# Optimization experiments

Hardware: AMD Instinct MI355X
Metric: run time of the kernel (lower is better)

## Reference

```python
import jax, jax.numpy as jnp
import numpy as np

B, L, C = 8, 1_000_000, 4


def _spiral_size(length: int) -> int:
    # size = round(sqrt(L / (pi/4 * 0.7)) / 2) * 2 + 1  (odd, size^2 >= L)
    s = np.sqrt(length / (np.pi / 4.0 * 0.7))
    return int(np.round(s / 2.0)) * 2 + 1


def _spiral_perm(size: int, length: int):
    """Grid slot index for each signal position (first `length` of argsort(phi2))."""
    PI = jnp.float32(np.pi)
    rnge = jnp.arange(size, dtype=jnp.float32) - size / 2.0 + 0.5
    x1, x2 = jnp.meshgrid(rnge, rnge)  # 'xy' indexing, same as tf.meshgrid default
    r = jnp.sqrt(x1 * x1 + x2 * x2)
    phi = jnp.arccos(x1 / r)                      # NaN at center (0/0)
    phi = jnp.where(jnp.isnan(phi), 0.0, phi)
    phi = phi * jnp.sign(x2)
    phi = phi + jnp.where((x2 == 0.0) & (x1 < 0.0), PI, 0.0)
    phi2 = jnp.round(r) * 2.0 * PI + phi          # spiral ordering key
    return jnp.argsort(phi2.reshape(-1))[:length]


def setup_inputs() -> dict:
    key = jax.random.key(0)
    return {"inputs": jax.random.normal(key, (B, L, C), dtype=jnp.float32)}


def reference(inputs):
    b, l, c = inputs.shape
    size = _spiral_size(l)
    perm = _spiral_perm(size, l)  # [l] unique grid slots
    # One-pass scatter of the signal into the dense size*size spiral grid
    grid = jnp.zeros((b, size * size, c), dtype=inputs.dtype).at[:, perm, :].set(inputs)
    return grid.reshape(b, size, size, c)
```

## Files before the change

kernel.cpp:

```cpp
#include <hip/hip_runtime.h>
#include <cstdint>

#define SIZE 1349
#define HALF 674
#define N2 (SIZE*SIZE)
#define LSIG 1000000
#define NB 8
#define GRID_RINGS 954
#define RANK_RINGS 600
#define CAP 5376
#define MBUCKET 2048

__device__ __forceinline__ int isqrt_i(int n) {
    int s = (int)sqrtf((float)n);
    while (s > 0 && s * s > n) s--;
    while ((s + 1) * (s + 1) <= n) s++;
    return s;
}

__device__ __forceinline__ int row_interval(int k, int y, int* xlo, int* xhi) {
    if (k == 0) { if (y == 0) { *xhi = 0; return 1; } return 0; }
    int yy = y * y;
    int B = k * (k + 1) - yy;
    if (B < 0) return 0;
    int h = isqrt_i(B);
    if (h > HALF) h = HALF;
    int A = k * (k - 1) + 1 - yy;
    *xhi = h;
    if (A <= 0) return 1;
    int f = isqrt_i(A);
    int lo = (f * f == A) ? f : f + 1;
    if (lo > h) return 0;
    *xlo = lo;
    return 2;
}

__device__ __forceinline__ uint32_t rowcnt(int k, int y) {
    int lo, hi;
    int kind = row_interval(k, y, &lo, &hi);
    if (kind == 0) return 0u;
    if (kind == 1) return (uint32_t)(2 * hi + 1);
    return (uint32_t)(2 * (hi - lo + 1));
}

__global__ void k_prep1(uint32_t* __restrict__ ringCount) {
    __shared__ uint32_t red[256];
    int k = blockIdx.x, t = threadIdx.x;
    int ymaxv = min(k, HALF);
    int nrows = 2 * ymaxv + 1;
    uint32_t s = 0;
    for (int i = t; i < nrows; i += 256) s += rowcnt(k, i - ymaxv);
    red[t] = s;
    __syncthreads();
    for (int d = 128; d > 0; d >>= 1) { if (t < d) red[t] += red[t + d]; __syncthreads(); }
    if (t == 0) ringCount[k] = red[0];
}

__global__ void k_prep2(const uint32_t* __restrict__ ringCount,
                        uint32_t* __restrict__ ringOffset,
                        uint32_t* __restrict__ nthresh) {
    __shared__ uint32_t s[1024];
    int t = threadIdx.x;
    uint32_t mine = (t < RANK_RINGS) ? ringCount[t] : 0u;
    s[t] = mine;
    __syncthreads();
    for (int d = 1; d < 1024; d <<= 1) {
        uint32_t x = (t >= d) ? s[t - d] : 0u;
        __syncthreads();
        s[t] += x;
        __syncthreads();
    }
    if (t < RANK_RINGS) ringOffset[t] = s[t] - mine;
    if (t >= 2 && t < RANK_RINGS && s[t - 1] >= LSIG && s[t - 2] < LSIG)
        *nthresh = (uint32_t)(t * (t - 1) + 1);
}

__device__ __forceinline__ int bucket_of(uint32_t kb, float tt) {
    const float PI_F = 3.14159265358979323846f;
    const float SC = 325.94932f;
    float p2 = __uint_as_float(kb);
    float u = (p2 - tt) + PI_F;
    int b = (int)(u * SC);
    return min(max(b, 0), MBUCKET - 1);
}

template<int PHASE>
__device__ __forceinline__ void enum_ring(int k, int ymaxv, float tt, int t,
                                          uint32_t* cnt, uint32_t* boff, uint64_t* T) {
#pragma clang fp contract(off)
    const float PI_F = 3.14159265358979323846f;
    int ntask = 2 * (ymaxv + 1);
    for (int task = t; task < ntask; task += 1024) {
        int y = task >> 1, side = task & 1;
        int xlo = 0, xhi = 0;
        int kind = row_interval(k, y, &xlo, &xhi);
        if (kind == 0) continue;
        int xs, xe;
        if (side == 0) {
            xs = -xhi; xe = (kind == 1) ? -1 : -xlo;
            if (xe < xs) continue;
        } else {
            xs = (kind == 1) ? 0 : xlo; xe = xhi;
        }
        for (int x = xs; x <= xe; ++x) {
            uint32_t kp, kn = 0;
            if (y == 0) {
                float phi = (x < 0) ? PI_F : 0.0f;
                kp = __float_as_uint(tt + phi);
            } else {
                int nn = x * x + y * y;
                float rr = sqrtf((float)nn);
                float q = (float)x / rr;
                float ac = (float)::acos((double)q);
                kp = __float_as_uint(tt + ac);
                kn = __float_as_uint(tt - ac);
            }
            uint32_t gx = (uint32_t)(x + HALF);
            uint32_t gp = (uint32_t)(y + HALF) * SIZE + gx;
            int bp = bucket_of(kp, tt);
            if (PHASE == 0) atomicAdd(&cnt[bp], 1u);
            else { uint32_t p = atomicAdd(&boff[bp], 1u); T[p] = ((uint64_t)kp << 32) | gp; }
            if (y > 0) {
                uint32_t gn = (uint32_t)(HALF - y) * SIZE + gx;
                int bn = bucket_of(kn, tt);
                if (PHASE == 0) atomicAdd(&cnt[bn], 1u);
                else { uint32_t p = atomicAdd(&boff[bn], 1u); T[p] = ((uint64_t)kn << 32) | gn; }
            }
        }
    }
}

__global__ __launch_bounds__(1024) void k_rank(const uint32_t* __restrict__ ringOffset,
                                               const uint32_t* __restrict__ ringCount,
                                               uint32_t* __restrict__ rank) {
#pragma clang fp contract(off)
    __shared__ uint64_t T[CAP];
    __shared__ uint32_t cnt[MBUCKET];
    __shared__ uint32_t boff[MBUCKET];
    __shared__ uint32_t ps[1024];
    const float PI_F = 3.14159265358979323846f;
    int k = (RANK_RINGS - 1) - blockIdx.x;
    int t = threadIdx.x;
    uint32_t off = ringOffset[k];
    if (off >= LSIG) return;
    if (k == 0) { if (t == 0) rank[HALF * SIZE + HALF] = 0u; return; }
    int ymaxv = min(k, HALF);
    int n = (int)ringCount[k];
    float tt = (2.0f * (float)k) * PI_F;

    cnt[2 * t] = 0u; cnt[2 * t + 1] = 0u;
    __syncthreads();

    enum_ring<0>(k, ymaxv, tt, t, cnt, boff, T);
    __syncthreads();

    uint32_t c0 = cnt[2 * t], c1 = cnt[2 * t + 1];
    uint32_t s = c0 + c1;
    ps[t] = s;
    __syncthreads();
    for (int d = 1; d < 1024; d <<= 1) {
        uint32_t x = (t >= d) ? ps[t - d] : 0u;
        __syncthreads();
        ps[t] += x;
        __syncthreads();
    }
    uint32_t excl = ps[t] - s;
    boff[2 * t] = excl;
    boff[2 * t + 1] = excl + c0;
    __syncthreads();

    enum_ring<1>(k, ymaxv, tt, t, cnt, boff, T);
    __syncthreads();

    for (int i = t; i < n; i += 1024) {
        uint64_t v = T[i];
        uint32_t kb = (uint32_t)(v >> 32);
        int b = bucket_of(kb, tt);
        uint32_t end = boff[b];
        uint32_t start = end - cnt[b];
        uint32_t c = 0;
        for (uint32_t j = start; j < end; ++j) c += (T[j] < v) ? 1u : 0u;
        rank[(uint32_t)v] = off + start + c;
    }
}

typedef float vfloat4 __attribute__((ext_vector_type(4)));

#define TW 32
#define TH 8

__global__ __launch_bounds__(256) void k_gather(const vfloat4* __restrict__ in,
                                                const uint32_t* __restrict__ rank,
                                                const uint32_t* __restrict__ nthresh,
                                                vfloat4* __restrict__ out) {
    int tx = threadIdx.x & (TW - 1);
    int ty = threadIdx.x >> 5;
    int col = blockIdx.x * TW + tx;
    int row = blockIdx.y * TH + ty;
    int b = blockIdx.z;
    if (col >= SIZE || row >= SIZE) return;
    int g = row * SIZE + col;
    int dx = col - HALF, dy = row - HALF;
    uint32_t n = (uint32_t)(dx * dx + dy * dy);
    uint32_t q = 0xFFFFFFFFu;
    if (n < *nthresh) q = rank[g];
    if (q < LSIG) {
        vfloat4 v = in[b * LSIG + (int)q];
        __builtin_nontemporal_store(v, &out[b * N2 + g]);
    } else {
        vfloat4 z = {0.f, 0.f, 0.f, 0.f};
        __builtin_nontemporal_store(z, &out[b * N2 + g]);
    }
}

extern "C" void kernel_launch(void* const* d_in, const int* in_sizes, int n_in,
                              void* d_out, int out_size, void* d_ws, size_t ws_size,
                              hipStream_t stream) {
    const float* in = (const float*)d_in[0];
    float* out = (float*)d_out;
    uint8_t* ws = (uint8_t*)d_ws;

    constexpr size_t RANK_OFF   = 0;
    constexpr size_t COUNT_OFF  = 7279616;
    constexpr size_t OFFSET_OFF = COUNT_OFF + 4096;
    constexpr size_t THRESH_OFF = OFFSET_OFF + 4096;

    uint32_t* rank       = (uint32_t*)(ws + RANK_OFF);
    uint32_t* ringCount  = (uint32_t*)(ws + COUNT_OFF);
    uint32_t* ringOffset = (uint32_t*)(ws + OFFSET_OFF);
    uint32_t* nthresh    = (uint32_t*)(ws + THRESH_OFF);

    k_prep1<<<RANK_RINGS, 256, 0, stream>>>(ringCount);
    k_prep2<<<1, 1024, 0, stream>>>(ringCount, ringOffset, nthresh);
    k_rank<<<RANK_RINGS, 1024, 0, stream>>>(ringOffset, ringCount, rank);

    dim3 gb((SIZE + TW - 1) / TW, (SIZE + TH - 1) / TH, NB);
    k_gather<<<gb, 256, 0, stream>>>((const vfloat4*)in, rank, nthresh, (vfloat4*)out);
}
```

Measured before the change: 371.7 us.

## Precompute ring offsets at compile time and enumerate each ring once

Ring counts and offsets are now computed with constexpr templates into a constant table, which removes the two prep kernels and their launches, and the live-ring count and radius threshold become compile-time constants. k_rank walks the ring points once, appending to LDS with a wave-aggregated atomic instead of the old count pass plus fill pass. The top of the circle is enumerated by column to balance per-thread work. Points are scattered into buckets in a global T2 buffer, and ranks are counted by scanning that global copy. The gather tile shape also changes to 16x16. The global bucket scan may cost more than the old LDS scan.

```diff
diff --git a/kernel.cpp b/kernel.cpp
--- a/kernel.cpp
+++ b/kernel.cpp
@@ -1,15 +1,70 @@
 #include <hip/hip_runtime.h>
 #include <cstdint>
+#include <utility>
 
 #define SIZE 1349
 #define HALF 674
 #define N2 (SIZE*SIZE)
 #define LSIG 1000000
 #define NB 8
-#define GRID_RINGS 954
-#define RANK_RINGS 600
+#define NRINGS 601
 #define CAP 5376
 #define MBUCKET 2048
+
+constexpr long long isqrt_c(long long n) {
+    if (n <= 0) return 0;
+    long long x = 1;
+    while (x * x <= n) x <<= 1;
+    long long r = 0;
+    for (long long b = x; b > 0; b >>= 1) { long long c = r + b; if (c * c <= n) r = c; }
+    return r;
+}
+constexpr uint32_t rowcnt_c(int k, int y) {
+    if (k == 0) return (y == 0) ? 1u : 0u;
+    long long yy = (long long)y * y;
+    long long Bv = (long long)k * (k + 1) - yy;
+    if (Bv < 0) return 0u;
+    long long h = isqrt_c(Bv); if (h > HALF) h = HALF;
+    long long Av = (long long)k * (k - 1) + 1 - yy;
+    if (Av <= 0) return (uint32_t)(2 * h + 1);
+    long long f = isqrt_c(Av);
+    long long lo = (f * f == Av) ? f : f + 1;
+    if (lo > h) return 0u;
+    return (uint32_t)(2 * (h - lo + 1));
+}
+constexpr uint32_t ringcnt_c(int k) {
+    int ym = (k < HALF) ? k : HALF;
+    uint32_t s = 0;
+    for (int y = -ym; y <= ym; ++y) s += rowcnt_c(k, y);
+    return s;
+}
+template<int K> struct RC { static constexpr uint32_t v = ringcnt_c(K); };
+template<int K> struct OF { static constexpr uint32_t v = OF<K - 1>::v + RC<K - 1>::v; };
+template<>      struct OF<0> { static constexpr uint32_t v = 0u; };
+
+struct OffArr { uint32_t a[NRINGS]; };
+template<int... I>
+constexpr OffArr mkoff(std::integer_sequence<int, I...>) { return {{ OF<I>::v... }}; }
+
+constexpr OffArr HOFF = mkoff(std::make_integer_sequence<int, NRINGS>{});
+
+constexpr int klive_c() {
+    for (int k = 0; k < NRINGS; ++k) if (HOFF.a[k] >= LSIG) return k;
+    return NRINGS;
+}
+constexpr int KLIVE = klive_c();
+constexpr uint32_t NTHRESH = (uint32_t)((long long)KLIVE * (KLIVE - 1) + 1);
+constexpr uint32_t maxcnt_c() {
+    uint32_t m = 0;
+    for (int k = 0; k < KLIVE; ++k) { uint32_t c = HOFF.a[k + 1] - HOFF.a[k]; if (c > m) m = c; }
+    return m;
+}
+static_assert(KLIVE < NRINGS - 1, "ring table too small");
+static_assert(KLIVE <= HALF, "ymax clamp assumption broken");
+static_assert(maxcnt_c() <= CAP, "CAP too small");
+static_assert(HOFF.a[KLIVE] < LSIG + CAP, "T2 sizing");
+
+__device__ __constant__ OffArr RING_OFF = mkoff(std::make_integer_sequence<int, NRINGS>{});
 
 __device__ __forceinline__ int isqrt_i(int n) {
     int s = (int)sqrtf((float)n);
@@ -35,46 +90,6 @@
     return 2;
 }
 
-__device__ __forceinline__ uint32_t rowcnt(int k, int y) {
-    int lo, hi;
-    int kind = row_interval(k, y, &lo, &hi);
-    if (kind == 0) return 0u;
-    if (kind == 1) return (uint32_t)(2 * hi + 1);
-    return (uint32_t)(2 * (hi - lo + 1));
-}
-
-__global__ void k_prep1(uint32_t* __restrict__ ringCount) {
-    __shared__ uint32_t red[256];
-    int k = blockIdx.x, t = threadIdx.x;
-    int ymaxv = min(k, HALF);
-    int nrows = 2 * ymaxv + 1;
-    uint32_t s = 0;
-    for (int i = t; i < nrows; i += 256) s += rowcnt(k, i - ymaxv);
-    red[t] = s;
-    __syncthreads();
-    for (int d = 128; d > 0; d >>= 1) { if (t < d) red[t] += red[t + d]; __syncthreads(); }
-    if (t == 0) ringCount[k] = red[0];
-}
-
-__global__ void k_prep2(const uint32_t* __restrict__ ringCount,
-                        uint32_t* __restrict__ ringOffset,
-                        uint32_t* __restrict__ nthresh) {
-    __shared__ uint32_t s[1024];
-    int t = threadIdx.x;
-    uint32_t mine = (t < RANK_RINGS) ? ringCount[t] : 0u;
-    s[t] = mine;
-    __syncthreads();
-    for (int d = 1; d < 1024; d <<= 1) {
-        uint32_t x = (t >= d) ? s[t - d] : 0u;
-        __syncthreads();
-        s[t] += x;
-        __syncthreads();
-    }
-    if (t < RANK_RINGS) ringOffset[t] = s[t] - mine;
-    if (t >= 2 && t < RANK_RINGS && s[t - 1] >= LSIG && s[t - 2] < LSIG)
-        *nthresh = (uint32_t)(t * (t - 1) + 1);
-}
-
 __device__ __forceinline__ int bucket_of(uint32_t kb, float tt) {
     const float PI_F = 3.14159265358979323846f;
     const float SC = 325.94932f;
@@ -84,74 +99,95 @@
     return min(max(b, 0), MBUCKET - 1);
 }
 
-template<int PHASE>
-__device__ __forceinline__ void enum_ring(int k, int ymaxv, float tt, int t,
-                                          uint32_t* cnt, uint32_t* boff, uint64_t* T) {
+__device__ __forceinline__ uint32_t lds_append(uint32_t* nT) {
+    unsigned long long m = __ballot(1);
+    int lane = threadIdx.x & 63;
+    int leader = __ffsll(m) - 1;
+    uint32_t base = 0;
+    if (lane == leader) base = atomicAdd(nT, (uint32_t)__popcll(m));
+    base = __shfl(base, leader);
+    return base + (uint32_t)__popcll(m & ((1ull << lane) - 1ull));
+}
+
+__device__ __forceinline__ void emit(int k, int x, int y, float tt,
+                                     uint64_t* T, uint32_t* cnt, uint32_t* nT) {
 #pragma clang fp contract(off)
     const float PI_F = 3.14159265358979323846f;
-    int ntask = 2 * (ymaxv + 1);
-    for (int task = t; task < ntask; task += 1024) {
-        int y = task >> 1, side = task & 1;
-        int xlo = 0, xhi = 0;
-        int kind = row_interval(k, y, &xlo, &xhi);
-        if (kind == 0) continue;
-        int xs, xe;
-        if (side == 0) {
-            xs = -xhi; xe = (kind == 1) ? -1 : -xlo;
-            if (xe < xs) continue;
-        } else {
-            xs = (kind == 1) ? 0 : xlo; xe = xhi;
-        }
-        for (int x = xs; x <= xe; ++x) {
-            uint32_t kp, kn = 0;
-            if (y == 0) {
-                float phi = (x < 0) ? PI_F : 0.0f;
-                kp = __float_as_uint(tt + phi);
-            } else {
-                int nn = x * x + y * y;
-                float rr = sqrtf((float)nn);
-                float q = (float)x / rr;
-                float ac = (float)::acos((double)q);
-                kp = __float_as_uint(tt + ac);
-                kn = __float_as_uint(tt - ac);
-            }
-            uint32_t gx = (uint32_t)(x + HALF);
-            uint32_t gp = (uint32_t)(y + HALF) * SIZE + gx;
-            int bp = bucket_of(kp, tt);
-            if (PHASE == 0) atomicAdd(&cnt[bp], 1u);
-            else { uint32_t p = atomicAdd(&boff[bp], 1u); T[p] = ((uint64_t)kp << 32) | gp; }
-            if (y > 0) {
-                uint32_t gn = (uint32_t)(HALF - y) * SIZE + gx;
-                int bn = bucket_of(kn, tt);
-                if (PHASE == 0) atomicAdd(&cnt[bn], 1u);
-                else { uint32_t p = atomicAdd(&boff[bn], 1u); T[p] = ((uint64_t)kn << 32) | gn; }
-            }
-        }
-    }
-}
-
-__global__ __launch_bounds__(1024) void k_rank(const uint32_t* __restrict__ ringOffset,
-                                               const uint32_t* __restrict__ ringCount,
-                                               uint32_t* __restrict__ rank) {
+    uint32_t kp, kn = 0;
+    if (y == 0) {
+        float phi = (x < 0) ? PI_F : 0.0f;
+        kp = __float_as_uint(tt + phi);
+    } else {
+        int nn = x * x + y * y;
+        float rr = sqrtf((float)nn);
+        float q = (float)x / rr;
+        float ac = (float)::acos((double)q);
+        kp = __float_as_uint(tt + ac);
+        kn = __float_as_uint(tt - ac);
+    }
+    uint32_t gx = (uint32_t)(x + HALF);
+    uint32_t gp = (uint32_t)(y + HALF) * SIZE + gx;
+    uint32_t p = lds_append(nT);
+    T[p] = ((uint64_t)kp << 32) | gp;
+    atomicAdd(&cnt[bucket_of(kp, tt)], 1u);
+    if (y > 0) {
+        uint32_t gn = (uint32_t)(HALF - y) * SIZE + gx;
+        uint32_t p2 = lds_append(nT);
+        T[p2] = ((uint64_t)kn << 32) | gn;
+        atomicAdd(&cnt[bucket_of(kn, tt)], 1u);
+    }
+}
+
+__global__ __launch_bounds__(1024) void k_rank(uint32_t* __restrict__ rank,
+                                               uint64_t* __restrict__ T2) {
 #pragma clang fp contract(off)
     __shared__ uint64_t T[CAP];
     __shared__ uint32_t cnt[MBUCKET];
     __shared__ uint32_t boff[MBUCKET];
     __shared__ uint32_t ps[1024];
+    __shared__ uint32_t nT;
     const float PI_F = 3.14159265358979323846f;
-    int k = (RANK_RINGS - 1) - blockIdx.x;
+    int k = (KLIVE - 1) - (int)blockIdx.x;
     int t = threadIdx.x;
-    uint32_t off = ringOffset[k];
-    if (off >= LSIG) return;
     if (k == 0) { if (t == 0) rank[HALF * SIZE + HALF] = 0u; return; }
-    int ymaxv = min(k, HALF);
-    int n = (int)ringCount[k];
+    uint32_t off = RING_OFF.a[k];
+    int n = (int)(RING_OFF.a[k + 1] - off);
     float tt = (2.0f * (float)k) * PI_F;
 
     cnt[2 * t] = 0u; cnt[2 * t + 1] = 0u;
-    __syncthreads();
-
-    enum_ring<0>(k, ymaxv, tt, t, cnt, boff, T);
+    if (t == 0) nT = 0u;
+    __syncthreads();
+
+    int capy = (k >= 32) ? (k - 8) : (k + 1);
+    int Bk = k * (k + 1), Ak = k * (k - 1) + 1;
+    int nmain = 2 * capy;
+    int w = 0, ncap = 0;
+    if (capy <= k) { w = isqrt_i(Bk - capy * capy); ncap = 2 * w + 1; }
+    int ntot = nmain + ncap;
+    for (int task = t; task < ntot; task += 1024) {
+        if (task < nmain) {
+            int y = task >> 1, side = task & 1;
+            int xlo = 0, xhi = 0;
+            int kind = row_interval(k, y, &xlo, &xhi);
+            if (kind == 0) continue;
+            int xs, xe;
+            if (side == 0) { xs = -xhi; xe = (kind == 1) ? -1 : -xlo; if (xe < xs) continue; }
+            else          { xs = (kind == 1) ? 0 : xlo; xe = xhi; }
+            for (int x = xs; x <= xe; ++x) emit(k, x, y, tt, T, cnt, &nT);
+        } else {
+            int x = (task - nmain) - w;
+            int xx = x * x;
+            int yhi = isqrt_i(Bk - xx);
+            int aa = Ak - xx;
+            int ylo = capy;
+            if (aa > 0) {
+                int f = isqrt_i(aa);
+                int lo = (f * f == aa) ? f : f + 1;
+                if (lo > ylo) ylo = lo;
+            }
+            for (int y = ylo; y <= yhi; ++y) emit(k, x, y, tt, T, cnt, &nT);
+        }
+    }
     __syncthreads();
 
     uint32_t c0 = cnt[2 * t], c1 = cnt[2 * t + 1];
@@ -169,41 +205,45 @@
     boff[2 * t + 1] = excl + c0;
     __syncthreads();
 
-    enum_ring<1>(k, ymaxv, tt, t, cnt, boff, T);
-    __syncthreads();
-
+    uint64_t* __restrict__ T2r = T2 + off;
     for (int i = t; i < n; i += 1024) {
         uint64_t v = T[i];
-        uint32_t kb = (uint32_t)(v >> 32);
-        int b = bucket_of(kb, tt);
+        int b = bucket_of((uint32_t)(v >> 32), tt);
+        uint32_t p = atomicAdd(&boff[b], 1u);
+        T2r[p] = v;
+    }
+    __syncthreads();
+
+    for (int i = t; i < n; i += 1024) {
+        uint64_t v = T[i];
+        int b = bucket_of((uint32_t)(v >> 32), tt);
         uint32_t end = boff[b];
         uint32_t start = end - cnt[b];
         uint32_t c = 0;
-        for (uint32_t j = start; j < end; ++j) c += (T[j] < v) ? 1u : 0u;
+        for (uint32_t j = start; j < end; ++j) c += (T2r[j] < v) ? 1u : 0u;
         rank[(uint32_t)v] = off + start + c;
     }
 }
 
 typedef float vfloat4 __attribute__((ext_vector_type(4)));
 
-#define TW 32
-#define TH 8
+#define TW 16
+#define TH 16
 
 __global__ __launch_bounds__(256) void k_gather(const vfloat4* __restrict__ in,
                                                 const uint32_t* __restrict__ rank,
-                                                const uint32_t* __restrict__ nthresh,
                                                 vfloat4* __restrict__ out) {
     int tx = threadIdx.x & (TW - 1);
-    int ty = threadIdx.x >> 5;
+    int ty = threadIdx.x / TW;
     int col = blockIdx.x * TW + tx;
     int row = blockIdx.y * TH + ty;
     int b = blockIdx.z;
     if (col >= SIZE || row >= SIZE) return;
     int g = row * SIZE + col;
     int dx = col - HALF, dy = row - HALF;
-    uint32_t n = (uint32_t)(dx * dx + dy * dy);
+    uint32_t nn = (uint32_t)(dx * dx + dy * dy);
     uint32_t q = 0xFFFFFFFFu;
-    if (n < *nthresh) q = rank[g];
+    if (nn < NTHRESH) q = rank[g];
     if (q < LSIG) {
         vfloat4 v = in[b * LSIG + (int)q];
         __builtin_nontemporal_store(v, &out[b * N2 + g]);
@@ -220,20 +260,11 @@
     float* out = (float*)d_out;
     uint8_t* ws = (uint8_t*)d_ws;
 
-    constexpr size_t RANK_OFF   = 0;
-    constexpr size_t COUNT_OFF  = 7279616;
-    constexpr size_t OFFSET_OFF = COUNT_OFF + 4096;
-    constexpr size_t THRESH_OFF = OFFSET_OFF + 4096;
-
-    uint32_t* rank       = (uint32_t*)(ws + RANK_OFF);
-    uint32_t* ringCount  = (uint32_t*)(ws + COUNT_OFF);
-    uint32_t* ringOffset = (uint32_t*)(ws + OFFSET_OFF);
-    uint32_t* nthresh    = (uint32_t*)(ws + THRESH_OFF);
-
-    k_prep1<<<RANK_RINGS, 256, 0, stream>>>(ringCount);
-    k_prep2<<<1, 1024, 0, stream>>>(ringCount, ringOffset, nthresh);
-    k_rank<<<RANK_RINGS, 1024, 0, stream>>>(ringOffset, ringCount, rank);
+    uint32_t* rank = (uint32_t*)ws;
+    uint64_t* T2   = (uint64_t*)(ws + 16 * 1024 * 1024);
+
+    k_rank<<<KLIVE, 1024, 0, stream>>>(rank, T2);
 
     dim3 gb((SIZE + TW - 1) / TW, (SIZE + TH - 1) / TH, NB);
-    k_gather<<<gb, 256, 0, stream>>>((const vfloat4*)in, rank, nthresh, (vfloat4*)out);
-}
+    k_gather<<<gb, 256, 0, stream>>>((const vfloat4*)in, rank, (vfloat4*)out);
+}
```

Measured after the change: 407.1 us. +9.5%, slower.
